# Kernel optimization log

Measured on AMD Instinct MI355X. Metric: run time of the kernel, lower is better.

The kernel has to match this reference:

```python
import jax, jax.numpy as jnp
import numpy as np

IN_F = 2048
OUT_F = 2048
GRID = 5
BATCH = 16384

def setup_inputs() -> dict:
    key = jax.random.key(0)
    kx, kb, ks = jax.random.split(key, 3)
    x = jax.random.normal(kx, (BATCH, IN_F), dtype=jnp.float32)
    # kaiming_uniform_(a=sqrt(5)) on [out, in]: bound = sqrt(6/((1+5)*in)) = 1/sqrt(in)
    bound = 1.0 / np.sqrt(IN_F)
    base_weight = jax.random.uniform(kb, (OUT_F, IN_F), minval=-bound, maxval=bound, dtype=jnp.float32)
    spline_weights = jax.random.uniform(ks, (OUT_F, IN_F, GRID), minval=-0.1, maxval=0.1, dtype=jnp.float32)
    return {"x": x, "base_weight": base_weight, "spline_weights": spline_weights}

def reference(x, base_weight, spline_weights):
    # base path: SiLU then linear (no bias)
    base_out = jnp.einsum('bi,oi->bo', jax.nn.silu(x), base_weight)
    # RBF spline basis over fixed grid in [-1, 1]
    grid = jnp.linspace(-1.0, 1.0, GRID, dtype=x.dtype)  # [g]
    basis = jnp.exp(-((x[..., None] - grid) ** 2) * 5.0)  # [b, i, g]
    spline_out = jnp.einsum('big,oig->bo', basis, spline_weights)
    return base_out + spline_out
```

## Files before the change

kernel.cpp:

```cpp
#include <hip/hip_runtime.h>
#include <hip/hip_bf16.h>
#include <cstdint>
#include <cstddef>


#define KIN 2048
#define NOUT 2048
#define BATCH 16384
#define KEXP 12288
#define NKT 192

typedef __bf16 bf16x8 __attribute__((ext_vector_type(8)));
typedef float f32x4 __attribute__((ext_vector_type(4)));
typedef unsigned short u16x4 __attribute__((ext_vector_type(4)));

__device__ __forceinline__ unsigned short f2bf(float f) {
    union { float f; uint32_t u; } v; v.f = f;
    return (unsigned short)((v.u + 0x7FFFu + ((v.u >> 16) & 1u)) >> 16);
}

__device__ __forceinline__ void load_lds16(const void* gptr, void* lptr) {
    __builtin_amdgcn_global_load_lds(
        (const __attribute__((address_space(1))) unsigned int*)gptr,
        (__attribute__((address_space(3))) unsigned int*)lptr,
        16, 0, 0);
}

__global__ __launch_bounds__(256)
void expand_a(const float* __restrict__ X, __bf16* __restrict__ Aexp)
{
    const int idx = blockIdx.x * 256 + threadIdx.x;
    const int row = idx >> 9;
    const int g   = idx & 511;
    const f32x4 xv = *(const f32x4*)(X + (size_t)row * KIN + g * 4);
    __bf16 o[24];
    #pragma unroll
    for (int e = 0; e < 4; ++e) {
        const float xf = xv[e];
        #pragma unroll
        for (int c = 0; c < 5; ++c) {
            const float d = xf - (-1.0f + 0.5f * (float)c);
            o[e * 6 + c] = (__bf16)__expf(-5.0f * d * d);
        }
        o[e * 6 + 5] = (__bf16)(xf / (1.0f + __expf(-xf)));
    }
    __bf16* dst = Aexp + (size_t)row * KEXP + g * 24;
    #pragma unroll
    for (int q = 0; q < 3; ++q) {
        bf16x8 v;
        #pragma unroll
        for (int t = 0; t < 8; ++t) v[t] = o[q * 8 + t];
        *(bf16x8*)(dst + q * 8) = v;
    }
}

__global__ __launch_bounds__(256)
void expand_w(const float* __restrict__ BW, const float* __restrict__ SW,
              __bf16* __restrict__ Wexp)
{
    const int idx = blockIdx.x * 256 + threadIdx.x;
    const int orow = idx >> 9;
    const int g    = idx & 511;
    const int i0   = g * 4;
    const float* sb = SW + ((size_t)orow * KIN + i0) * 5;
    const f32x4 bw = *(const f32x4*)(BW + (size_t)orow * KIN + i0);
    float sw[20];
    #pragma unroll
    for (int q = 0; q < 5; ++q) {
        const f32x4 v = *(const f32x4*)(sb + q * 4);
        sw[q * 4 + 0] = v.x; sw[q * 4 + 1] = v.y; sw[q * 4 + 2] = v.z; sw[q * 4 + 3] = v.w;
    }
    __bf16 o[24];
    #pragma unroll
    for (int e = 0; e < 4; ++e) {
        #pragma unroll
        for (int c = 0; c < 5; ++c) o[e * 6 + c] = (__bf16)sw[e * 5 + c];
        o[e * 6 + 5] = (__bf16)bw[e];
    }
    __bf16* dst = Wexp + (size_t)orow * KEXP + g * 24;
    #pragma unroll
    for (int q = 0; q < 3; ++q) {
        bf16x8 v;
        #pragma unroll
        for (int t = 0; t < 8; ++t) v[t] = o[q * 8 + t];
        *(bf16x8*)(dst + q * 8) = v;
    }
}

__global__ __launch_bounds__(512, 2)
void gemm8(const __bf16* __restrict__ A, const __bf16* __restrict__ W,
           float* __restrict__ OUT)
{
    __shared__ __align__(16) __bf16 LDS[65536];
    __bf16* LA = LDS;
    __bf16* LB = LDS + 32768;

    const int tid  = threadIdx.x;
    const int lane = tid & 63;
    const int wave = tid >> 6;
    const int r    = lane & 15;
    const int quad = lane >> 4;
    const int wm   = wave >> 2;
    const int wn   = wave & 3;

    const int bid0 = blockIdx.x;
    const int bid  = (bid0 & 7) * 64 + (bid0 >> 3);
    const int mt  = bid >> 3;
    const int nt  = bid & 7;
    const int m0  = mt * 256;
    const int n0  = nt * 256;

    const int c0   = tid;
    const int c1   = tid + 512;
    const int row0 = c0 >> 2, row1 = c1 >> 2;
    const int j0   = (c0 & 3) ^ ((c0 >> 3) & 3);
    const int j1   = (c1 & 3) ^ ((c1 >> 3) & 3);
    const __bf16* srcA0 = A + (size_t)(m0 + row0) * KEXP + j0 * 8;
    const __bf16* srcA1 = A + (size_t)(m0 + row1) * KEXP + j1 * 8;
    const __bf16* srcB0 = W + (size_t)(n0 + row0) * KEXP + j0 * 8;
    const __bf16* srcB1 = W + (size_t)(n0 + row1) * KEXP + j1 * 8;

    const int dst0 = wave * 512;
    const int dst1 = 4096 + wave * 512;

    const int swz = (quad ^ ((r >> 1) & 3)) * 8;
    const __bf16* a_rd = LA + (wm * 128 + r) * 32 + swz;
    const __bf16* b_rd = LB + (wn * 64 + r) * 32 + swz;

    f32x4 acc[8][4];
    #pragma unroll
    for (int i = 0; i < 8; ++i)
        #pragma unroll
        for (int j = 0; j < 4; ++j)
            acc[i][j] = (f32x4){0.0f, 0.0f, 0.0f, 0.0f};

    bf16x8 af[4], bf[4];

#define BARX() asm volatile("s_barrier" ::: "memory")
#define VM6()  asm volatile("s_waitcnt vmcnt(6)" ::: "memory")

#define STAGE_A(buf, kh, kt) do { \
    const size_t ko = (size_t)(kt) * 64 + (kh) * 32; \
    load_lds16(srcA0 + ko, LA + ((buf) * 2 + (kh)) * 8192 + dst0); \
    load_lds16(srcA1 + ko, LA + ((buf) * 2 + (kh)) * 8192 + dst1); } while (0)

#define STAGE_B(buf, kh, kt) do { \
    const size_t ko = (size_t)(kt) * 64 + (kh) * 32; \
    load_lds16(srcB0 + ko, LB + ((buf) * 2 + (kh)) * 8192 + dst0); \
    load_lds16(srcB1 + ko, LB + ((buf) * 2 + (kh)) * 8192 + dst1); } while (0)

#define READ_A(buf, ks, a) do { \
    const __bf16* p_ = a_rd + ((buf) * 2 + (ks)) * 8192 + (a) * 2048; \
    af[0] = *(const bf16x8*)(p_); \
    af[1] = *(const bf16x8*)(p_ + 512); \
    af[2] = *(const bf16x8*)(p_ + 1024); \
    af[3] = *(const bf16x8*)(p_ + 1536); } while (0)

#define READ_B(buf, ks) do { \
    const __bf16* p_ = b_rd + ((buf) * 2 + (ks)) * 8192; \
    bf[0] = *(const bf16x8*)(p_); \
    bf[1] = *(const bf16x8*)(p_ + 512); \
    bf[2] = *(const bf16x8*)(p_ + 1024); \
    bf[3] = *(const bf16x8*)(p_ + 1536); } while (0)

#define MFMA_Q(a) do { \
    __builtin_amdgcn_s_setprio(1); \
    _Pragma("unroll") \
    for (int mi_ = 0; mi_ < 4; ++mi_) { \
        _Pragma("unroll") \
        for (int nj_ = 0; nj_ < 4; ++nj_) \
            acc[(a) * 4 + mi_][nj_] = __builtin_amdgcn_mfma_f32_16x16x32_bf16( \
                af[mi_], bf[nj_], acc[(a) * 4 + mi_][nj_], 0, 0, 0); \
    } \
    __builtin_amdgcn_s_setprio(0); } while (0)

    STAGE_B(0, 0, 0); STAGE_A(0, 0, 0); STAGE_B(0, 1, 0); STAGE_A(0, 1, 0);
    STAGE_B(1, 0, 1); STAGE_A(1, 0, 1); STAGE_B(1, 1, 1);
    VM6();
    BARX();

    for (int t = 0; t < 96; ++t) {
        const int kt1 = 2 * t + 1;
        const int sA  = (2 * t + 2 < NKT) ? 2 * t + 2 : NKT - 1;
        const int sB  = (2 * t + 3 < NKT) ? 2 * t + 3 : NKT - 1;
        READ_A(0, 0, 0); READ_B(0, 0);
        STAGE_A(1, 1, kt1);
        BARX(); MFMA_Q(0); BARX();
        READ_A(0, 0, 1);
        STAGE_B(0, 0, sA);
        BARX(); MFMA_Q(1); BARX();
        READ_A(0, 1, 1); READ_B(0, 1);
        STAGE_A(0, 0, sA);
        BARX(); MFMA_Q(1); BARX();
        READ_A(0, 1, 0);
        STAGE_B(0, 1, sA);
        VM6();
        BARX(); MFMA_Q(0); BARX();
        READ_A(1, 0, 0); READ_B(1, 0);
        STAGE_A(0, 1, sA);
        BARX(); MFMA_Q(0); BARX();
        READ_A(1, 0, 1);
        STAGE_B(1, 0, sB);
        BARX(); MFMA_Q(1); BARX();
        READ_A(1, 1, 1); READ_B(1, 1);
        STAGE_A(1, 0, sB);
        BARX(); MFMA_Q(1); BARX();
        READ_A(1, 1, 0);
        STAGE_B(1, 1, sB);
        VM6();
        BARX(); MFMA_Q(0); BARX();
    }

    #pragma unroll
    for (int fi = 0; fi < 8; ++fi) {
        #pragma unroll
        for (int nj = 0; nj < 4; ++nj) {
            const int col  = n0 + wn * 64 + nj * 16 + r;
            const int rowb = m0 + wm * 128 + fi * 16 + quad * 4;
            #pragma unroll
            for (int reg = 0; reg < 4; ++reg)
                OUT[(size_t)(rowb + reg) * NOUT + col] = acc[fi][nj][reg];
        }
    }
#undef BARX
#undef VM6
#undef STAGE_A
#undef STAGE_B
#undef READ_A
#undef READ_B
#undef MFMA_Q
}

#define BM 128
#define BN 128
#define NF 16
#define BK 96
#define LDK 104

__global__ __launch_bounds__(256)
void kan_fused(const float* __restrict__ X, const float* __restrict__ BW,
               const float* __restrict__ SW, float* __restrict__ OUT)
{
    __shared__ __align__(16) unsigned short As[BM * LDK];
    __shared__ __align__(16) unsigned short Bs[BN * LDK];

    const int tid  = threadIdx.x;
    const int lane = tid & 63;
    const int wave = tid >> 6;
    const int mt = blockIdx.x >> 4;
    const int nt = blockIdx.x & 15;
    const int m0 = mt * BM;
    const int n0 = nt * BN;
    const int r    = lane & 15;
    const int quad = lane >> 4;
    const int wm = (wave & 1) * 64;
    const int wn = (wave >> 1) * 64;

    f32x4 acc[4][4];
    #pragma unroll
    for (int i = 0; i < 4; ++i)
        #pragma unroll
        for (int j = 0; j < 4; ++j)
            acc[i][j] = (f32x4){0.0f, 0.0f, 0.0f, 0.0f};

    for (int it = 0; it < KIN / NF; ++it) {
        const int i0 = it * NF;
        __syncthreads();
        #pragma unroll
        for (int s = 0; s < 2; ++s) {
            const int slot = tid + s * 256;
            const int row  = slot >> 2;
            const int fq   = slot & 3;
            const f32x4 xv = *(const f32x4*)(X + (size_t)(m0 + row) * KIN + i0 + fq * 4);
            unsigned short basv[20];
            unsigned short silv[4];
            #pragma unroll
            for (int e = 0; e < 4; ++e) {
                const float xf = xv[e];
                silv[e] = f2bf(xf / (1.0f + __expf(-xf)));
                #pragma unroll
                for (int c = 0; c < 5; ++c) {
                    const float d = xf - (-1.0f + 0.5f * (float)c);
                    basv[e * 5 + c] = f2bf(__expf(-5.0f * d * d));
                }
            }
            unsigned short* dst = As + row * LDK + fq * 20;
            #pragma unroll
            for (int q = 0; q < 5; ++q) {
                u16x4 v;
                v.x = basv[q * 4 + 0]; v.y = basv[q * 4 + 1];
                v.z = basv[q * 4 + 2]; v.w = basv[q * 4 + 3];
                *(u16x4*)(dst + q * 4) = v;
            }
            u16x4 sv;
            sv.x = silv[0]; sv.y = silv[1]; sv.z = silv[2]; sv.w = silv[3];
            *(u16x4*)(As + row * LDK + 80 + fq * 4) = sv;
        }
        {
            const int orow = tid >> 1;
            const int half = tid & 1;
            const float* sbase = SW + (size_t)(n0 + orow) * (KIN * 5) + i0 * 5 + half * 40;
            unsigned short* brow = Bs + orow * LDK + half * 40;
            #pragma unroll
            for (int p = 0; p < 10; ++p) {
                const f32x4 wv = *(const f32x4*)(sbase + p * 4);
                u16x4 v;
                v.x = f2bf(wv.x); v.y = f2bf(wv.y);
                v.z = f2bf(wv.z); v.w = f2bf(wv.w);
                *(u16x4*)(brow + p * 4) = v;
            }
        }
        #pragma unroll
        for (int s = 0; s < 2; ++s) {
            const int slot = tid + s * 256;
            const int row  = slot >> 2;
            const int fq   = slot & 3;
            const f32x4 wv = *(const f32x4*)(BW + (size_t)(n0 + row) * KIN + i0 + fq * 4);
            u16x4 v;
            v.x = f2bf(wv.x); v.y = f2bf(wv.y);
            v.z = f2bf(wv.z); v.w = f2bf(wv.w);
            *(u16x4*)(Bs + row * LDK + 80 + fq * 4) = v;
        }
        __syncthreads();
        #pragma unroll
        for (int ks = 0; ks < 3; ++ks) {
            bf16x8 af[4], bfr[4];
            #pragma unroll
            for (int mi = 0; mi < 4; ++mi)
                af[mi] = *(const bf16x8*)(As + (wm + mi * 16 + r) * LDK + ks * 32 + quad * 8);
            #pragma unroll
            for (int ni = 0; ni < 4; ++ni)
                bfr[ni] = *(const bf16x8*)(Bs + (wn + ni * 16 + r) * LDK + ks * 32 + quad * 8);
            #pragma unroll
            for (int mi = 0; mi < 4; ++mi)
                #pragma unroll
                for (int ni = 0; ni < 4; ++ni)
                    acc[mi][ni] = __builtin_amdgcn_mfma_f32_16x16x32_bf16(
                        af[mi], bfr[ni], acc[mi][ni], 0, 0, 0);
        }
    }
    #pragma unroll
    for (int mi = 0; mi < 4; ++mi) {
        #pragma unroll
        for (int ni = 0; ni < 4; ++ni) {
            const int col  = n0 + wn + ni * 16 + r;
            const int rowb = m0 + wm + mi * 16 + quad * 4;
            #pragma unroll
            for (int reg = 0; reg < 4; ++reg)
                OUT[(size_t)(rowb + reg) * NOUT + col] = acc[mi][ni][reg];
        }
    }
}

extern "C" void kernel_launch(void* const* d_in, const int* in_sizes, int n_in,
                              void* d_out, int out_size, void* d_ws, size_t ws_size,
                              hipStream_t stream) {
    const float* X  = (const float*)d_in[0];
    const float* BW = (const float*)d_in[1];
    const float* SW = (const float*)d_in[2];
    float* OUT = (float*)d_out;

    const size_t nA = (size_t)BATCH * KEXP;
    const size_t nW = (size_t)NOUT * KEXP;
    const size_t ws_need = (nA + nW) * sizeof(__bf16);

    if (ws_size >= ws_need) {
        __bf16* Aexp = (__bf16*)d_ws;
        __bf16* Wexp = Aexp + nA;
        expand_a<<<dim3(BATCH * 512 / 256), dim3(256), 0, stream>>>(X, Aexp);
        expand_w<<<dim3(NOUT * 512 / 256), dim3(256), 0, stream>>>(BW, SW, Wexp);
        gemm8<<<dim3(512), dim3(512), 0, stream>>>(Aexp, Wexp, OUT);
    } else {
        kan_fused<<<dim3(128 * 16), dim3(256), 0, stream>>>(X, BW, SW, OUT);
    }
}
```

Baseline: 995.8 us.

## Stage expanded rows in LDS for coalesced stores and cut exp calls via recurrence

The expand kernels now process one row per block, build the interleaved expanded row in shared memory, and then write it to global memory as fully coalesced 16-byte vectors, replacing the strided 48-byte-per-thread stores. The RBF basis in expand_a is computed with two exponentials plus a multiplicative recurrence using precomputed constants instead of five exponentials. The recurrence can amplify rounding error for large |x|, and each block now needs 24KB of LDS.

```diff
diff --git a/kernel.cpp b/kernel.cpp
--- a/kernel.cpp
+++ b/kernel.cpp
@@ -29,62 +29,89 @@
 __global__ __launch_bounds__(256)
 void expand_a(const float* __restrict__ X, __bf16* __restrict__ Aexp)
 {
-    const int idx = blockIdx.x * 256 + threadIdx.x;
-    const int row = idx >> 9;
-    const int g   = idx & 511;
-    const f32x4 xv = *(const f32x4*)(X + (size_t)row * KIN + g * 4);
-    __bf16 o[24];
-    #pragma unroll
-    for (int e = 0; e < 4; ++e) {
-        const float xf = xv[e];
-        #pragma unroll
-        for (int c = 0; c < 5; ++c) {
-            const float d = xf - (-1.0f + 0.5f * (float)c);
-            o[e * 6 + c] = (__bf16)__expf(-5.0f * d * d);
-        }
-        o[e * 6 + 5] = (__bf16)(xf / (1.0f + __expf(-xf)));
-    }
-    __bf16* dst = Aexp + (size_t)row * KEXP + g * 24;
-    #pragma unroll
-    for (int q = 0; q < 3; ++q) {
-        bf16x8 v;
-        #pragma unroll
-        for (int t = 0; t < 8; ++t) v[t] = o[q * 8 + t];
-        *(bf16x8*)(dst + q * 8) = v;
-    }
+    __shared__ __align__(16) __bf16 rowbuf[KEXP];
+    const int row = blockIdx.x;
+    const int tid = threadIdx.x;
+    const float* xrow = X + (size_t)row * KIN;
+
+    const float K0 = 42.521082000062783f;
+    const float K1 = 3.4903429574597902f;
+    const float K2 = 0.2865047968601901f;
+    const float K3 = 0.023517745856009107f;
+
+    #pragma unroll
+    for (int s = 0; s < 2; ++s) {
+        const f32x4 xv = *(const f32x4*)(xrow + (s * 256 + tid) * 4);
+        float o[24];
+        #pragma unroll
+        for (int e = 0; e < 4; ++e) {
+            const float xf = xv[e];
+            const float d0 = xf + 1.0f;
+            float b = __expf(-5.0f * d0 * d0);
+            const float s5 = __expf(5.0f * xf);
+            o[e * 6 + 0] = b;
+            b *= s5 * K0; o[e * 6 + 1] = b;
+            b *= s5 * K1; o[e * 6 + 2] = b;
+            b *= s5 * K2; o[e * 6 + 3] = b;
+            b *= s5 * K3; o[e * 6 + 4] = b;
+            o[e * 6 + 5] = xf / (1.0f + __expf(-xf));
+        }
+        __bf16* dst = rowbuf + (s * 1024 + tid * 4) * 6;
+        #pragma unroll
+        for (int q = 0; q < 3; ++q) {
+            bf16x8 v;
+            #pragma unroll
+            for (int t = 0; t < 8; ++t) v[t] = (__bf16)o[q * 8 + t];
+            *(bf16x8*)(dst + q * 8) = v;
+        }
+    }
+    __syncthreads();
+    bf16x8* out = (bf16x8*)(Aexp + (size_t)row * KEXP);
+    const bf16x8* lsrc = (const bf16x8*)rowbuf;
+    #pragma unroll
+    for (int t = 0; t < 6; ++t)
+        out[tid + t * 256] = lsrc[tid + t * 256];
 }
 
 __global__ __launch_bounds__(256)
 void expand_w(const float* __restrict__ BW, const float* __restrict__ SW,
               __bf16* __restrict__ Wexp)
 {
-    const int idx = blockIdx.x * 256 + threadIdx.x;
-    const int orow = idx >> 9;
-    const int g    = idx & 511;
-    const int i0   = g * 4;
-    const float* sb = SW + ((size_t)orow * KIN + i0) * 5;
-    const f32x4 bw = *(const f32x4*)(BW + (size_t)orow * KIN + i0);
-    float sw[20];
-    #pragma unroll
-    for (int q = 0; q < 5; ++q) {
-        const f32x4 v = *(const f32x4*)(sb + q * 4);
-        sw[q * 4 + 0] = v.x; sw[q * 4 + 1] = v.y; sw[q * 4 + 2] = v.z; sw[q * 4 + 3] = v.w;
-    }
-    __bf16 o[24];
-    #pragma unroll
-    for (int e = 0; e < 4; ++e) {
-        #pragma unroll
-        for (int c = 0; c < 5; ++c) o[e * 6 + c] = (__bf16)sw[e * 5 + c];
-        o[e * 6 + 5] = (__bf16)bw[e];
-    }
-    __bf16* dst = Wexp + (size_t)orow * KEXP + g * 24;
-    #pragma unroll
-    for (int q = 0; q < 3; ++q) {
-        bf16x8 v;
-        #pragma unroll
-        for (int t = 0; t < 8; ++t) v[t] = o[q * 8 + t];
-        *(bf16x8*)(dst + q * 8) = v;
-    }
+    __shared__ __align__(16) __bf16 rowbuf[KEXP];
+    const int orow = blockIdx.x;
+    const int tid  = threadIdx.x;
+
+    #pragma unroll
+    for (int s = 0; s < 2; ++s) {
+        const int i0 = s * 1024 + tid * 4;
+        const float* sb = SW + ((size_t)orow * KIN + i0) * 5;
+        const f32x4 bw = *(const f32x4*)(BW + (size_t)orow * KIN + i0);
+        float sw[20];
+        #pragma unroll
+        for (int q = 0; q < 5; ++q) {
+            const f32x4 v = *(const f32x4*)(sb + q * 4);
+            sw[q * 4 + 0] = v.x; sw[q * 4 + 1] = v.y;
+            sw[q * 4 + 2] = v.z; sw[q * 4 + 3] = v.w;
+        }
+        __bf16* dst = rowbuf + (size_t)i0 * 6;
+        #pragma unroll
+        for (int q = 0; q < 3; ++q) {
+            bf16x8 v;
+            #pragma unroll
+            for (int t = 0; t < 8; ++t) {
+                const int e = (q * 8 + t) / 6;
+                const int c = (q * 8 + t) % 6;
+                v[t] = (c < 5) ? (__bf16)sw[e * 5 + c] : (__bf16)bw[e];
+            }
+            *(bf16x8*)(dst + q * 8) = v;
+        }
+    }
+    __syncthreads();
+    bf16x8* out = (bf16x8*)(Wexp + (size_t)orow * KEXP);
+    const bf16x8* lsrc = (const bf16x8*)rowbuf;
+    #pragma unroll
+    for (int t = 0; t < 6; ++t)
+        out[tid + t * 256] = lsrc[tid + t * 256];
 }
 
 __global__ __launch_bounds__(512, 2)
@@ -367,8 +394,8 @@
     if (ws_size >= ws_need) {
         __bf16* Aexp = (__bf16*)d_ws;
         __bf16* Wexp = Aexp + nA;
-        expand_a<<<dim3(BATCH * 512 / 256), dim3(256), 0, stream>>>(X, Aexp);
-        expand_w<<<dim3(NOUT * 512 / 256), dim3(256), 0, stream>>>(BW, SW, Wexp);
+        expand_a<<<dim3(BATCH), dim3(256), 0, stream>>>(X, Aexp);
+        expand_w<<<dim3(NOUT), dim3(256), 0, stream>>>(BW, SW, Wexp);
         gemm8<<<dim3(512), dim3(512), 0, stream>>>(Aexp, Wexp, OUT);
     } else {
         kan_fused<<<dim3(128 * 16), dim3(256), 0, stream>>>(X, BW, SW, OUT);
```

After: 970.4 us. 2.6% less time.
